# Optimization experiments

Hardware: AMD Instinct MI355X
Metric: run time of the kernel (lower is better)

Reference implementation:

```python
import jax, jax.numpy as jnp
import numpy as np

N = 100000      # nodes
E = 640000      # edges
IN = 100        # in_channels
OUT = 128       # out_channels
H, D = 4, 32    # heads, per-head dim (OUT = H*D)
MSG, TOUT, ETD, NET = 16, 100, 8, 4
EDGE_COLS = MSG + TOUT + 2        # 118 raw edge_attr columns
EDIM = (MSG - 1) + ETD + TOUT + 2 # 125 processed edge feature dim
SCALE = 1.0 / np.sqrt(D)


def _lin(k, fi, fo):
    return (jax.random.normal(k, (fi, fo), jnp.float32) / np.sqrt(fi)).astype(jnp.float32)


def setup_inputs() -> dict:
    key = jax.random.key(0)
    ks = jax.random.split(key, 24)
    x = jax.random.normal(ks[0], (N, IN), jnp.float32)
    edge_index = jax.random.randint(ks[1], (2, E), 0, N, dtype=jnp.int32)
    ea = jax.random.normal(ks[2], (E, EDGE_COLS), jnp.float32)
    etype = jax.random.randint(ks[3], (E,), 0, NET).astype(jnp.float32)
    edge_attr = ea.at[:, 3].set(etype)
    emb = jax.random.normal(ks[4], (NET, ETD), jnp.float32)
    inp = {"x": x, "edge_index": edge_index, "edge_attr": edge_attr, "emb": emb}
    # conv1: in=IN, conv2: in=OUT; lin_edge has no bias (PyG default)
    for i, fi in ((1, IN), (2, OUT)):
        base = 5 + (i - 1) * 8
        inp[f"w{i}q"] = _lin(ks[base + 0], fi, OUT)
        inp[f"b{i}q"] = jnp.zeros((OUT,), jnp.float32)
        inp[f"w{i}k"] = _lin(ks[base + 1], fi, OUT)
        inp[f"b{i}k"] = jnp.zeros((OUT,), jnp.float32)
        inp[f"w{i}v"] = _lin(ks[base + 2], fi, OUT)
        inp[f"b{i}v"] = jnp.zeros((OUT,), jnp.float32)
        inp[f"w{i}e"] = _lin(ks[base + 3], EDIM, OUT)
        inp[f"w{i}s"] = _lin(ks[base + 4], fi, OUT)
        inp[f"b{i}s"] = jnp.zeros((OUT,), jnp.float32)
    return inp


def _seg_softmax(logits, seg, n):
    # logits: [E, H], softmax over edges sharing the same target node
    m = jax.ops.segment_max(logits, seg, num_segments=n)      # [N, H]
    ex = jnp.exp(logits - m[seg])
    s = jax.ops.segment_sum(ex, seg, num_segments=n)          # [N, H]
    return ex / (s[seg] + 1e-16)


def _tconv(x, src, dst, e, wq, bq, wk, bk, wv, bv, we, ws, bs):
    n = x.shape[0]
    q = (x @ wq + bq)[dst].reshape(-1, H, D)   # gather targets
    k = (x @ wk + bk)[src].reshape(-1, H, D)   # gather sources
    v = (x @ wv + bv)[src].reshape(-1, H, D)
    ee = (e @ we).reshape(-1, H, D)            # per-edge projection
    alpha = jnp.sum(q * (k + ee), axis=-1) * SCALE          # [E, H]
    a = _seg_softmax(alpha, dst, n)                          # scatter-softmax
    msg = (v + ee) * a[..., None]                            # [E, H, D]
    out = jax.ops.segment_sum(msg, dst, num_segments=n).reshape(n, H * D)
    return out + x @ ws + bs                                 # root/skip connection


def reference(x, edge_index, edge_attr, emb,
              w1q, b1q, w1k, b1k, w1v, b1v, w1e, w1s, b1s,
              w2q, b2q, w2k, b2k, w2v, b2v, w2e, w2s, b2s):
    src, dst = edge_index[0], edge_index[1]
    cont = edge_attr[:, :3]
    etype = edge_attr[:, 3].astype(jnp.int32)
    rest = edge_attr[:, 4:]
    e = jnp.concatenate([cont, rest, emb[etype]], axis=-1)   # [E, EDIM]
    h = jax.nn.relu(_tconv(x, src, dst, e, w1q, b1q, w1k, b1k, w1v, b1v, w1e, w1s, b1s))
    return _tconv(h, src, dst, e, w2q, b2q, w2k, b2k, w2v, b2v, w2e, w2s, b2s)
```

## Files before the change

### kernel.cpp

```cpp
#include <hip/hip_runtime.h>

#define NN 100000
#define NE 640000
#define OUTF 128
#define K1 100
#define KE 118
#define KPAD 128
#define ASTR 136
#define ATT_SCALE 0.17677669529663687f
#define NSCANB 391

typedef __attribute__((ext_vector_type(8))) short short8;
typedef __attribute__((ext_vector_type(4))) float f32x4;

__device__ __forceinline__ unsigned short f2bf(float f) {
    unsigned u = __float_as_uint(f);
    u += 0x7FFFu + ((u >> 16) & 1u);
    return (unsigned short)(u >> 16);
}
__device__ __forceinline__ float bf2f(unsigned short h) {
    return __uint_as_float(((unsigned)h) << 16);
}

__global__ void prep_weights(
    const float* __restrict__ w1q, const float* __restrict__ w1k,
    const float* __restrict__ w1v, const float* __restrict__ w1s,
    const float* __restrict__ w2q, const float* __restrict__ w2k,
    const float* __restrict__ w2v, const float* __restrict__ w2s,
    const float* __restrict__ we1, const float* __restrict__ we2,
    const float* __restrict__ emb,
    const float* __restrict__ b1q, const float* __restrict__ b1k,
    const float* __restrict__ b1v, const float* __restrict__ b1s,
    const float* __restrict__ b2q, const float* __restrict__ b2k,
    const float* __restrict__ b2v, const float* __restrict__ b2s,
    unsigned short* __restrict__ WT1, unsigned short* __restrict__ WT2,
    unsigned short* __restrict__ WmT1, unsigned short* __restrict__ WmT2,
    float* __restrict__ bias1, float* __restrict__ bias2)
{
    int idx = blockIdx.x * blockDim.x + threadIdx.x;
    int stride = gridDim.x * blockDim.x;
    for (int i = idx; i < 512 * KPAD; i += stride) {
        int col = i >> 7, k = i & 127;
        int which = col >> 7, c = col & 127;
        const float* s1 = (which == 0) ? w1q : (which == 1) ? w1k : (which == 2) ? w1v : w1s;
        const float* s2 = (which == 0) ? w2q : (which == 1) ? w2k : (which == 2) ? w2v : w2s;
        float v1 = (k < K1) ? s1[k * OUTF + c] : 0.f;
        float v2 = s2[k * OUTF + c];
        WT1[i] = f2bf(v1); WT2[i] = f2bf(v2);
    }
    for (int i = idx; i < OUTF * KPAD; i += stride) {
        int col = i >> 7, k = i & 127;
        float v1 = 0.f, v2 = 0.f;
        if (k < 3)                 { v1 = we1[k * OUTF + col];       v2 = we2[k * OUTF + col]; }
        else if (k >= 4 && k < KE) { v1 = we1[(k - 1) * OUTF + col]; v2 = we2[(k - 1) * OUTF + col]; }
        else if (k >= KE && k < KE + 4) {
            int t = k - KE;
            #pragma unroll
            for (int r = 0; r < 8; r++) {
                float ev = emb[t * 8 + r];
                v1 += ev * we1[(117 + r) * OUTF + col];
                v2 += ev * we2[(117 + r) * OUTF + col];
            }
        }
        WmT1[i] = f2bf(v1); WmT2[i] = f2bf(v2);
    }
    for (int i = idx; i < 512; i += stride) {
        int which = i >> 7, c = i & 127;
        const float* sb1 = (which == 0) ? b1q : (which == 1) ? b1k : (which == 2) ? b1v : b1s;
        const float* sb2 = (which == 0) ? b2q : (which == 1) ? b2k : (which == 2) ? b2v : b2s;
        bias1[i] = sb1[c]; bias2[i] = sb2[c];
    }
}

__global__ __launch_bounds__(256) void convert_ea(const float* __restrict__ EA,
                                                  unsigned short* __restrict__ EAb)
{
    int lane = threadIdx.x & 63;
    int gw = (int)((blockIdx.x * (size_t)blockDim.x + threadIdx.x) >> 6);
    int nW = (gridDim.x * blockDim.x) >> 6;
    int k = lane * 2;
    for (int e = gw; e < NE; e += nW) {
        const float* row = EA + (size_t)e * KE;
        float2 v = make_float2(0.f, 0.f);
        if (k < KE) v = *(const float2*)(row + k);
        int et = (int)row[3];
        if (lane == 1) v.y = 0.f;
        int oh = KE + et;
        if (k == oh)     v.x = 1.f;
        if (k + 1 == oh) v.y = 1.f;
        unsigned pv = (unsigned)f2bf(v.x) | ((unsigned)f2bf(v.y) << 16);
        *(unsigned*)(EAb + (size_t)e * 128 + k) = pv;
    }
}

__global__ void hist_kernel(const int* __restrict__ dstI, int* __restrict__ cnt) {
    int e = blockIdx.x * 256 + threadIdx.x;
    if (e < NE) atomicAdd(&cnt[dstI[e]], 1);
}
__global__ void scan1(const int* __restrict__ cnt, int* __restrict__ S1, int* __restrict__ bsum) {
    __shared__ int sd[256];
    int t = blockIdx.x * 256 + threadIdx.x;
    sd[threadIdx.x] = (t < NN) ? cnt[t] : 0;
    __syncthreads();
    for (int off = 1; off < 256; off <<= 1) {
        int x = (threadIdx.x >= off) ? sd[threadIdx.x - off] : 0;
        __syncthreads();
        sd[threadIdx.x] += x;
        __syncthreads();
    }
    if (t < NN) S1[t] = sd[threadIdx.x];
    if (threadIdx.x == 255) bsum[blockIdx.x] = sd[255];
}
__global__ void scan2(const int* __restrict__ bsum, int* __restrict__ boff) {
    __shared__ int sd[512];
    int t = threadIdx.x;
    sd[t] = (t < NSCANB) ? bsum[t] : 0;
    __syncthreads();
    for (int off = 1; off < 512; off <<= 1) {
        int x = (t >= off) ? sd[t - off] : 0;
        __syncthreads();
        sd[t] += x;
        __syncthreads();
    }
    if (t < NSCANB) boff[t] = (t == 0) ? 0 : sd[t - 1];
}
__global__ void scan3(const int* __restrict__ S1, const int* __restrict__ boff,
                      const int* __restrict__ cnt,
                      int* __restrict__ row_start, int* __restrict__ cursor) {
    int t = blockIdx.x * 256 + threadIdx.x;
    if (t < NN) {
        int incl = S1[t] + boff[t >> 8];
        row_start[t + 1] = incl;
        cursor[t] = incl - cnt[t];
        if (t == 0) row_start[0] = 0;
    }
}
__global__ void scatter_csr(const int* __restrict__ srcI, const int* __restrict__ dstI,
                            int* __restrict__ cursor,
                            int* __restrict__ csr_src, int* __restrict__ csr_eid) {
    int e = blockIdx.x * 256 + threadIdx.x;
    if (e < NE) {
        int j = atomicAdd(&cursor[dstI[e]], 1);
        csr_src[j] = srcI[e];
        csr_eid[j] = e;
    }
}

__global__ __launch_bounds__(256) void node_mfma(
    const float* __restrict__ X, int ldx, int Kdim, int relu, int n,
    const unsigned short* __restrict__ WT, const float* __restrict__ bias,
    float* __restrict__ Qp, unsigned short* __restrict__ KVp, float* __restrict__ Hp)
{
    __shared__ unsigned short Alds[128][ASTR];
    int tid = threadIdx.x;
    int rowbase = (blockIdx.x >> 2) * 128;
    int nb = blockIdx.x & 3;

    for (int idx = tid; idx < 128 * 68; idx += 256) {
        int r = idx / 68, kv = idx % 68;
        int k = kv * 2;
        float2 v = make_float2(0.f, 0.f);
        int gr = rowbase + r;
        if (gr < n && k < Kdim) v = *(const float2*)(X + (size_t)gr * ldx + k);
        if (relu) { v.x = fmaxf(v.x, 0.f); v.y = fmaxf(v.y, 0.f); }
        unsigned pv = (unsigned)f2bf(v.x) | ((unsigned)f2bf(v.y) << 16);
        *(unsigned*)&Alds[r][k] = pv;
    }
    __syncthreads();

    int lane = tid & 63, wid = tid >> 6;
    int wm = wid >> 1, wn = wid & 1;
    int l15 = lane & 15, l4 = lane >> 4;

    f32x4 acc[4][4];
    #pragma unroll
    for (int mf = 0; mf < 4; mf++)
        #pragma unroll
        for (int nf = 0; nf < 4; nf++)
            acc[mf][nf] = (f32x4){0.f, 0.f, 0.f, 0.f};

    const unsigned short* wbase = WT + (size_t)(nb * 128 + wn * 64 + l15) * KPAD + l4 * 8;
    #pragma unroll
    for (int ks = 0; ks < 4; ks++) {
        short8 af[4], bfr[4];
        #pragma unroll
        for (int mf = 0; mf < 4; mf++)
            af[mf] = *(const short8*)&Alds[wm * 64 + mf * 16 + l15][ks * 32 + l4 * 8];
        #pragma unroll
        for (int nf = 0; nf < 4; nf++)
            bfr[nf] = *(const short8*)(wbase + (size_t)nf * 16 * KPAD + ks * 32);
        #pragma unroll
        for (int mf = 0; mf < 4; mf++)
            #pragma unroll
            for (int nf = 0; nf < 4; nf++)
                acc[mf][nf] = __builtin_amdgcn_mfma_f32_16x16x32_bf16(af[mf], bfr[nf], acc[mf][nf], 0, 0, 0);
    }
    __syncthreads();

    if (nb == 1 || nb == 2) {
        #pragma unroll
        for (int nf = 0; nf < 4; nf++) {
            int col = wn * 64 + nf * 16 + l15;
            float bv = bias[nb * 128 + col];
            #pragma unroll
            for (int mf = 0; mf < 4; mf++)
                #pragma unroll
                for (int rr = 0; rr < 4; rr++)
                    Alds[wm * 64 + mf * 16 + l4 * 4 + rr][col] = f2bf(acc[mf][nf][rr] + bv);
        }
        __syncthreads();
        int off = (nb == 1) ? 0 : 128;
        #pragma unroll
        for (int it = 0; it < 8; it++) {
            int idx = it * 256 + tid;
            int row = idx >> 4, c8 = (idx & 15) * 8;
            if (rowbase + row < n) {
                uint4 v = *(const uint4*)&Alds[row][c8];
                *(uint4*)(KVp + (size_t)(rowbase + row) * 256 + off + c8) = v;
            }
        }
    } else {
        float* Yp = (nb == 0) ? Qp : Hp;
        float scale = (nb == 0) ? ATT_SCALE : 1.f;
        float (*Sf)[68] = (float (*)[68])Alds;
        #pragma unroll
        for (int h = 0; h < 2; h++) {
            if (wn == h) {
                #pragma unroll
                for (int nf = 0; nf < 4; nf++) {
                    int col = wn * 64 + nf * 16 + l15;
                    float bv = bias[nb * 128 + col];
                    #pragma unroll
                    for (int mf = 0; mf < 4; mf++)
                        #pragma unroll
                        for (int rr = 0; rr < 4; rr++)
                            Sf[wm * 64 + mf * 16 + l4 * 4 + rr][nf * 16 + l15] =
                                (acc[mf][nf][rr] + bv) * scale;
                }
            }
            __syncthreads();
            #pragma unroll
            for (int it = 0; it < 8; it++) {
                int idx = it * 256 + tid;
                int row = idx >> 4, c4 = (idx & 15) * 4;
                if (rowbase + row < n) {
                    float4 v = *(const float4*)&Sf[row][c4];
                    *(float4*)(Yp + (size_t)(rowbase + row) * OUTF + h * 64 + c4) = v;
                }
            }
            if (h == 0) __syncthreads();
        }
    }
}

__global__ __launch_bounds__(256) void edge_mfma_one(
    const unsigned short* __restrict__ EAb,
    const unsigned short* __restrict__ WmT,
    unsigned short* EEc)
{
    __shared__ unsigned short Tlds[64][ASTR];
    int tid = threadIdx.x;
    int lane = tid & 63, w = tid >> 6;
    int e0 = blockIdx.x * 64;
    int l15 = lane & 15, l4 = lane >> 4;
    int rbase = w * 16;

    short8 af[4];
    #pragma unroll
    for (int ks = 0; ks < 4; ks++)
        af[ks] = *(const short8*)(EAb + (size_t)(e0 + rbase + l15) * 128 + ks * 32 + l4 * 8);

    f32x4 acc[8];
    #pragma unroll
    for (int nf = 0; nf < 8; nf++) acc[nf] = (f32x4){0.f, 0.f, 0.f, 0.f};

    #pragma unroll
    for (int ks = 0; ks < 4; ks++) {
        short8 bfr[8];
        #pragma unroll
        for (int nf = 0; nf < 8; nf++)
            bfr[nf] = *(const short8*)(WmT + (size_t)(nf * 16 + l15) * KPAD + ks * 32 + l4 * 8);
        #pragma unroll
        for (int nf = 0; nf < 8; nf++)
            acc[nf] = __builtin_amdgcn_mfma_f32_16x16x32_bf16(af[ks], bfr[nf], acc[nf], 0, 0, 0);
    }

    #pragma unroll
    for (int nf = 0; nf < 8; nf++)
        #pragma unroll
        for (int rr = 0; rr < 4; rr++)
            Tlds[rbase + l4 * 4 + rr][nf * 16 + l15] = f2bf(acc[nf][rr]);
    #pragma unroll
    for (int it = 0; it < 4; it++) {
        int t2 = it * 64 + lane;
        int rid = t2 >> 4, c8 = (t2 & 15) * 8;
        uint4 v = *(const uint4*)&Tlds[rbase + rid][c8];
        *(uint4*)(EEc + ((size_t)(e0 + rbase + rid)) * 128 + c8) = v;
    }
}

__global__ __launch_bounds__(256) void attn_node(
    const float* __restrict__ Qp, const unsigned short* __restrict__ KVp,
    const unsigned short* __restrict__ EEc,
    const int* __restrict__ row_start, const int* __restrict__ csr_src,
    const int* __restrict__ csr_eid,
    const float* __restrict__ Hskip, float* __restrict__ Out)
{
    int lane = threadIdx.x & 63;
    int gw = (int)((blockIdx.x * (size_t)blockDim.x + threadIdx.x) >> 6);
    int nW = (gridDim.x * blockDim.x) >> 6;
    int c2 = lane * 2;

    for (int d = gw; d < NN; d += nW) {
        int rs = row_start[d], re = row_start[d + 1];
        float2 q = *(const float2*)(Qp + (size_t)d * OUTF + c2);
        float m = -3.4e38f, s = 0.f, a0 = 0.f, a1 = 0.f;

        int j0 = (rs < re) ? rs : 0;
        int sj = csr_src[j0];
        int ej = csr_eid[j0];
        unsigned kc = *(const unsigned*)(KVp + (size_t)sj * 256 + c2);
        unsigned vc = *(const unsigned*)(KVp + (size_t)sj * 256 + 128 + c2);
        unsigned ec = *(const unsigned*)(EEc + (size_t)ej * 128 + c2);

        for (int j = rs; j < re; j++) {
            int jn = (j + 1 < re) ? j + 1 : j;
            int sjn = csr_src[jn];
            int ejn = csr_eid[jn];
            unsigned kn = *(const unsigned*)(KVp + (size_t)sjn * 256 + c2);
            unsigned vn = *(const unsigned*)(KVp + (size_t)sjn * 256 + 128 + c2);
            unsigned en = *(const unsigned*)(EEc + (size_t)ejn * 128 + c2);

            float e0 = bf2f((unsigned short)(ec & 0xFFFFu));
            float e1 = bf2f((unsigned short)(ec >> 16));
            float k0 = bf2f((unsigned short)(kc & 0xFFFFu));
            float k1 = bf2f((unsigned short)(kc >> 16));
            float v0 = bf2f((unsigned short)(vc & 0xFFFFu));
            float v1 = bf2f((unsigned short)(vc >> 16));

            float t = q.x * (k0 + e0) + q.y * (k1 + e1);
            t += __shfl_xor(t, 1); t += __shfl_xor(t, 2);
            t += __shfl_xor(t, 4); t += __shfl_xor(t, 8);
            float alpha = t;
            float mn = fmaxf(m, alpha);
            float r = __expf(m - mn);
            float p = __expf(alpha - mn);
            s = s * r + p;
            a0 = a0 * r + p * (v0 + e0);
            a1 = a1 * r + p * (v1 + e1);
            m = mn;
            kc = kn; vc = vn; ec = en;
        }
        float inv = 1.f / (s + 1e-16f);
        float2 h = *(const float2*)(Hskip + (size_t)d * OUTF + c2);
        float2 o;
        o.x = a0 * inv + h.x;
        o.y = a1 * inv + h.y;
        *(float2*)(Out + (size_t)d * OUTF + c2) = o;
    }
}

extern "C" void kernel_launch(void* const* d_in, const int* in_sizes, int n_in,
                              void* d_out, int out_size, void* d_ws, size_t ws_size,
                              hipStream_t stream) {
    const float* x    = (const float*)d_in[0];
    const int*   ei   = (const int*)d_in[1];
    const float* ea   = (const float*)d_in[2];
    const float* emb  = (const float*)d_in[3];
    const float* w1q  = (const float*)d_in[4];  const float* b1q = (const float*)d_in[5];
    const float* w1k  = (const float*)d_in[6];  const float* b1k = (const float*)d_in[7];
    const float* w1v  = (const float*)d_in[8];  const float* b1v = (const float*)d_in[9];
    const float* w1e  = (const float*)d_in[10];
    const float* w1s  = (const float*)d_in[11]; const float* b1s = (const float*)d_in[12];
    const float* w2q  = (const float*)d_in[13]; const float* b2q = (const float*)d_in[14];
    const float* w2k  = (const float*)d_in[15]; const float* b2k = (const float*)d_in[16];
    const float* w2v  = (const float*)d_in[17]; const float* b2v = (const float*)d_in[18];
    const float* w2e  = (const float*)d_in[19];
    const float* w2s  = (const float*)d_in[20]; const float* b2s = (const float*)d_in[21];

    const int* srcI = ei;
    const int* dstI = ei + NE;

    float* Q = (float*)d_ws;
    unsigned short* KV = (unsigned short*)(Q + (size_t)NN * OUTF);
    float* H = (float*)(KV + (size_t)NN * 256);
    unsigned short* EE1 = (unsigned short*)(H + (size_t)NN * OUTF);
    unsigned short* EAb = EE1 + (size_t)NE * 128;
    int* csr_src   = (int*)(EAb + (size_t)NE * 128);
    int* csr_eid   = csr_src + NE;
    int* row_start = csr_eid + NE;
    int* cursor    = row_start + NN + 1;
    int* cnt       = cursor + NN;
    int* S1        = cnt + NN;
    int* bsum      = S1 + NN;
    int* boff      = bsum + NSCANB;
    unsigned short* WT1  = (unsigned short*)(boff + NSCANB + 1);
    unsigned short* WT2  = WT1 + 512 * KPAD;
    unsigned short* WmT1 = WT2 + 512 * KPAD;
    unsigned short* WmT2 = WmT1 + OUTF * KPAD;
    float* bias1 = (float*)(WmT2 + OUTF * KPAD);
    float* bias2 = bias1 + 512;

    prep_weights<<<128, 256, 0, stream>>>(w1q, w1k, w1v, w1s, w2q, w2k, w2v, w2s,
                                          w1e, w2e, emb,
                                          b1q, b1k, b1v, b1s, b2q, b2k, b2v, b2s,
                                          WT1, WT2, WmT1, WmT2, bias1, bias2);
    hipMemsetAsync(cnt, 0, (size_t)NN * sizeof(int), stream);
    hist_kernel<<<NE / 256, 256, 0, stream>>>(dstI, cnt);
    scan1<<<NSCANB, 256, 0, stream>>>(cnt, S1, bsum);
    scan2<<<1, 512, 0, stream>>>(bsum, boff);
    scan3<<<NSCANB, 256, 0, stream>>>(S1, boff, cnt, row_start, cursor);
    scatter_csr<<<NE / 256, 256, 0, stream>>>(srcI, dstI, cursor, csr_src, csr_eid);
    convert_ea<<<4096, 256, 0, stream>>>(ea, EAb);

    int ngrid = ((NN + 127) / 128) * 4;
    int egrid = NE / 64;

    node_mfma<<<ngrid, 256, 0, stream>>>(x, K1, K1, 0, NN, WT1, bias1, Q, KV, H);
    edge_mfma_one<<<egrid, 256, 0, stream>>>(EAb, WmT1, EE1);
    edge_mfma_one<<<egrid, 256, 0, stream>>>(EAb, WmT2, EAb);
    attn_node<<<2048, 256, 0, stream>>>(Q, KV, EE1, row_start, csr_src, csr_eid, H, H);

    node_mfma<<<ngrid, 256, 0, stream>>>(H, OUTF, OUTF, 1, NN, WT2, bias2, Q, KV, (float*)d_out);
    attn_node<<<2048, 256, 0, stream>>>(Q, KV, EAb, row_start, csr_src, csr_eid, (float*)d_out, (float*)d_out);
}
```

Baseline: 1.138 ms.

## Fuse edge-attr conversion and both edge projections into one dual-output kernel

Removes the separate convert_ea pass and merges the two per-layer edge projection kernels into one. Each block loads raw fp32 edge_attr rows into LDS, converts them to bf16 and inserts the edge-type one-hot there. It then reuses the same A fragments for both layers' weight matrices and writes EE1 and EE2. The goal is to stop writing the bf16 EAb buffer and reading it twice, which cuts a large amount of global memory traffic and one kernel launch. It needs a separate EE2 buffer instead of overwriting EAb in place. It also keeps more registers live and reuses the LDS tile for output staging.

```diff
diff --git a/kernel.cpp b/kernel.cpp
--- a/kernel.cpp
+++ b/kernel.cpp
@@ -72,27 +72,6 @@
     }
 }
 
-__global__ __launch_bounds__(256) void convert_ea(const float* __restrict__ EA,
-                                                  unsigned short* __restrict__ EAb)
-{
-    int lane = threadIdx.x & 63;
-    int gw = (int)((blockIdx.x * (size_t)blockDim.x + threadIdx.x) >> 6);
-    int nW = (gridDim.x * blockDim.x) >> 6;
-    int k = lane * 2;
-    for (int e = gw; e < NE; e += nW) {
-        const float* row = EA + (size_t)e * KE;
-        float2 v = make_float2(0.f, 0.f);
-        if (k < KE) v = *(const float2*)(row + k);
-        int et = (int)row[3];
-        if (lane == 1) v.y = 0.f;
-        int oh = KE + et;
-        if (k == oh)     v.x = 1.f;
-        if (k + 1 == oh) v.y = 1.f;
-        unsigned pv = (unsigned)f2bf(v.x) | ((unsigned)f2bf(v.y) << 16);
-        *(unsigned*)(EAb + (size_t)e * 128 + k) = pv;
-    }
-}
-
 __global__ void hist_kernel(const int* __restrict__ dstI, int* __restrict__ cnt) {
     int e = blockIdx.x * 256 + threadIdx.x;
     if (e < NE) atomicAdd(&cnt[dstI[e]], 1);
@@ -253,50 +232,73 @@
     }
 }
 
-__global__ __launch_bounds__(256) void edge_mfma_one(
-    const unsigned short* __restrict__ EAb,
-    const unsigned short* __restrict__ WmT,
-    unsigned short* EEc)
+__global__ __launch_bounds__(256) void edge_mfma_dual(
+    const float* __restrict__ EA,
+    const unsigned short* __restrict__ WmT1, const unsigned short* __restrict__ WmT2,
+    unsigned short* __restrict__ EE1, unsigned short* __restrict__ EE2)
 {
-    __shared__ unsigned short Tlds[64][ASTR];
+    __shared__ unsigned short Alds[64][ASTR];
+    __shared__ int et_lds[64];
     int tid = threadIdx.x;
+    int e0 = blockIdx.x * 64;
     int lane = tid & 63, w = tid >> 6;
-    int e0 = blockIdx.x * 64;
     int l15 = lane & 15, l4 = lane >> 4;
     int rbase = w * 16;
+
+    #pragma unroll 4
+    for (int it = 0; it < 16; it++) {
+        int idx = it * 256 + tid;
+        int r = idx >> 6, slot = idx & 63;
+        int k = slot * 2;
+        float2 v = make_float2(0.f, 0.f);
+        if (k < KE) v = *(const float2*)(EA + (size_t)(e0 + r) * KE + k);
+        if (slot == 1) { et_lds[r] = (int)v.y; v.y = 0.f; }
+        unsigned pv = (unsigned)f2bf(v.x) | ((unsigned)f2bf(v.y) << 16);
+        *(unsigned*)&Alds[r][k] = pv;
+    }
+    __syncthreads();
 
     short8 af[4];
     #pragma unroll
     for (int ks = 0; ks < 4; ks++)
-        af[ks] = *(const short8*)(EAb + (size_t)(e0 + rbase + l15) * 128 + ks * 32 + l4 * 8);
-
-    f32x4 acc[8];
+        af[ks] = *(const short8*)&Alds[rbase + l15][ks * 32 + l4 * 8];
+    int oh = KE + et_lds[rbase + l15];
     #pragma unroll
-    for (int nf = 0; nf < 8; nf++) acc[nf] = (f32x4){0.f, 0.f, 0.f, 0.f};
-
-    #pragma unroll
-    for (int ks = 0; ks < 4; ks++) {
-        short8 bfr[8];
+    for (int j = 0; j < 8; j++) {
+        int col = 96 + l4 * 8 + j;
+        if (col == oh) af[3][j] = 0x3F80;
+    }
+
+    auto do_layer = [&](const unsigned short* __restrict__ WmT, unsigned short* __restrict__ EEc) {
+        f32x4 acc[8];
+        #pragma unroll
+        for (int nf = 0; nf < 8; nf++) acc[nf] = (f32x4){0.f, 0.f, 0.f, 0.f};
+
+        #pragma unroll
+        for (int ks = 0; ks < 4; ks++) {
+            short8 bfr[8];
+            #pragma unroll
+            for (int nf = 0; nf < 8; nf++)
+                bfr[nf] = *(const short8*)(WmT + (size_t)(nf * 16 + l15) * KPAD + ks * 32 + l4 * 8);
+            #pragma unroll
+            for (int nf = 0; nf < 8; nf++)
+                acc[nf] = __builtin_amdgcn_mfma_f32_16x16x32_bf16(af[ks], bfr[nf], acc[nf], 0, 0, 0);
+        }
         #pragma unroll
         for (int nf = 0; nf < 8; nf++)
-            bfr[nf] = *(const short8*)(WmT + (size_t)(nf * 16 + l15) * KPAD + ks * 32 + l4 * 8);
-        #pragma unroll
-        for (int nf = 0; nf < 8; nf++)
-            acc[nf] = __builtin_amdgcn_mfma_f32_16x16x32_bf16(af[ks], bfr[nf], acc[nf], 0, 0, 0);
-    }
-
-    #pragma unroll
-    for (int nf = 0; nf < 8; nf++)
-        #pragma unroll
-        for (int rr = 0; rr < 4; rr++)
-            Tlds[rbase + l4 * 4 + rr][nf * 16 + l15] = f2bf(acc[nf][rr]);
-    #pragma unroll
-    for (int it = 0; it < 4; it++) {
-        int t2 = it * 64 + lane;
-        int rid = t2 >> 4, c8 = (t2 & 15) * 8;
-        uint4 v = *(const uint4*)&Tlds[rbase + rid][c8];
-        *(uint4*)(EEc + ((size_t)(e0 + rbase + rid)) * 128 + c8) = v;
-    }
+            #pragma unroll
+            for (int rr = 0; rr < 4; rr++)
+                Alds[rbase + l4 * 4 + rr][nf * 16 + l15] = f2bf(acc[nf][rr]);
+        #pragma unroll
+        for (int it = 0; it < 4; it++) {
+            int t2 = it * 64 + lane;
+            int rid = t2 >> 4, c8 = (t2 & 15) * 8;
+            uint4 v = *(const uint4*)&Alds[rbase + rid][c8];
+            *(uint4*)(EEc + ((size_t)(e0 + rbase + rid)) * 128 + c8) = v;
+        }
+    };
+    do_layer(WmT1, EE1);
+    do_layer(WmT2, EE2);
 }
 
 __global__ __launch_bounds__(256) void attn_node(
@@ -385,8 +387,8 @@
     unsigned short* KV = (unsigned short*)(Q + (size_t)NN * OUTF);
     float* H = (float*)(KV + (size_t)NN * 256);
     unsigned short* EE1 = (unsigned short*)(H + (size_t)NN * OUTF);
-    unsigned short* EAb = EE1 + (size_t)NE * 128;
-    int* csr_src   = (int*)(EAb + (size_t)NE * 128);
+    unsigned short* EE2 = EE1 + (size_t)NE * 128;
+    int* csr_src   = (int*)(EE2 + (size_t)NE * 128);
     int* csr_eid   = csr_src + NE;
     int* row_start = csr_eid + NE;
     int* cursor    = row_start + NN + 1;
@@ -411,16 +413,14 @@
     scan2<<<1, 512, 0, stream>>>(bsum, boff);
     scan3<<<NSCANB, 256, 0, stream>>>(S1, boff, cnt, row_start, cursor);
     scatter_csr<<<NE / 256, 256, 0, stream>>>(srcI, dstI, cursor, csr_src, csr_eid);
-    convert_ea<<<4096, 256, 0, stream>>>(ea, EAb);
 
     int ngrid = ((NN + 127) / 128) * 4;
     int egrid = NE / 64;
 
     node_mfma<<<ngrid, 256, 0, stream>>>(x, K1, K1, 0, NN, WT1, bias1, Q, KV, H);
-    edge_mfma_one<<<egrid, 256, 0, stream>>>(EAb, WmT1, EE1);
-    edge_mfma_one<<<egrid, 256, 0, stream>>>(EAb, WmT2, EAb);
+    edge_mfma_dual<<<egrid, 256, 0, stream>>>(ea, WmT1, WmT2, EE1, EE2);
     attn_node<<<2048, 256, 0, stream>>>(Q, KV, EE1, row_start, csr_src, csr_eid, H, H);
 
     node_mfma<<<ngrid, 256, 0, stream>>>(H, OUTF, OUTF, 1, NN, WT2, bias2, Q, KV, (float*)d_out);
-    attn_node<<<2048, 256, 0, stream>>>(Q, KV, EAb, row_start, csr_src, csr_eid, (float*)d_out, (float*)d_out);
-}
+    attn_node<<<2048, 256, 0, stream>>>(Q, KV, EE2, row_start, csr_src, csr_eid, (float*)d_out, (float*)d_out);
+}
```

Measured after the change: 1.123 ms. Within noise of the previous version (-1.3%).
